# Performance work log

Hardware: AMD Instinct MI355X
Metric: run time of the kernel (lower is better)

Reference implementation:

```python
import jax, jax.numpy as jnp
import numpy as np

B, T, C = 2, 2048, 1280
H, D = 10, 128  # n_head, head_dim (n_kv_head == n_head, so no repeat)
EPS = 1e-5
NEG = -1e9


def setup_inputs() -> dict:
    key = jax.random.key(0)
    ks = jax.random.split(key, 7)
    s = 0.02
    return {
        "x": jax.random.normal(ks[0], (B, T, C), jnp.float32),
        "cos": jax.random.normal(ks[1], (1, 1, T, D // 2), jnp.float32),
        "sin": jax.random.normal(ks[2], (1, 1, T, D // 2), jnp.float32),
        "Wq": jax.random.normal(ks[3], (C, C), jnp.float32) * s,
        "Wk": jax.random.normal(ks[4], (C, C), jnp.float32) * s,
        "Wv": jax.random.normal(ks[5], (C, C), jnp.float32) * s,
        "Wproj": jax.random.normal(ks[6], (C, C), jnp.float32) * s,
    }


def _rope(x, cos, sin):
    # x: [b,h,t,d]; split last dim in half
    x1, x2 = jnp.split(x, 2, axis=-1)
    y1 = x1 * cos + x2 * sin
    y2 = -x1 * sin + x2 * cos
    return jnp.concatenate([y1, y2], axis=-1)


def _rms_norm(x):
    mean = jnp.mean(x * x, axis=-1, keepdims=True)
    return x / jnp.sqrt(mean + EPS)


def reference(x, cos, sin, Wq, Wk, Wv, Wproj):
    b, t, c = x.shape
    # nn.Linear: y = x @ W.T; weights stored [out, in]
    q = (x @ Wq.T).reshape(b, t, H, D).transpose(0, 2, 1, 3)  # [b,h,t,d]
    k = (x @ Wk.T).reshape(b, t, H, D).transpose(0, 2, 1, 3)
    v = (x @ Wv.T).reshape(b, t, H, D).transpose(0, 2, 1, 3)
    q = _rms_norm(_rope(q, cos, sin))
    k = _rms_norm(_rope(k, cos, sin))
    scale = 1.0 / jnp.sqrt(jnp.float32(D))
    scores = jnp.einsum("bhqd,bhkd->bhqk", q, k) * scale
    mask = jnp.triu(jnp.ones((t, t), scores.dtype), k=1)  # 1 above diagonal
    scores = scores + mask * NEG
    attn = jax.nn.softmax(scores, axis=-1)
    y = jnp.einsum("bhqk,bhkd->bhqd", attn, v)
    y = y.transpose(0, 2, 1, 3).reshape(b, t, c)
    return y @ Wproj.T
```

## Files before the change

### kernel.cpp

```cpp
#include <hip/hip_runtime.h>
#include <hip/hip_bf16.h>

#define B_ 2
#define T_ 2048
#define C_ 1280
#define H_ 10
#define D_ 128
#define BT_ (B_*T_)

typedef __hip_bfloat16 bf16;
typedef __attribute__((ext_vector_type(8))) short short8;
typedef __attribute__((ext_vector_type(4))) float f32x4;

__device__ __forceinline__ float bf2f(bf16 v){ return __bfloat162float(v); }
__device__ __forceinline__ bf16  f2bf(float v){ return __float2bfloat16(v); }

struct alignas(8) bf4 { bf16 a,b,c,d; };

__device__ __forceinline__ void gl2lds(const bf16* g, bf16* l) {
    __builtin_amdgcn_global_load_lds(
        (const __attribute__((address_space(1))) void*)g,
        (__attribute__((address_space(3))) void*)l,
        16, 0, 0);
}

__global__ __launch_bounds__(256)
void cvtall(const float* __restrict__ x,  const float* __restrict__ w0,
            const float* __restrict__ w1, const float* __restrict__ w2,
            const float* __restrict__ w3, bf16* __restrict__ xb,
            bf16* __restrict__ wb)
{
    int bid = blockIdx.x;
    const float* s; bf16* d; int i;
    if (bid < 5120) {
        s = x; d = xb; i = (bid*256 + threadIdx.x)*4;
    } else {
        bid -= 5120;
        const int w = bid / 1600;
        const int r = bid % 1600;
        s = (w==0)?w0:(w==1)?w1:(w==2)?w2:w3;
        d = wb + (size_t)w*C_*C_;
        i = (r*256 + threadIdx.x)*4;
    }
    const float4 v = *(const float4*)(s + i);
    bf4 o = { f2bf(v.x), f2bf(v.y), f2bf(v.z), f2bf(v.w) };
    *(bf4*)(d + i) = o;
}

__global__ __launch_bounds__(256,4)
void gemm_qkv(const bf16* __restrict__ A, const bf16* __restrict__ Wb,
              bf16* __restrict__ q, bf16* __restrict__ k, bf16* __restrict__ vT,
              const float* __restrict__ cosp, const float* __restrict__ sinp)
{
    __shared__ __align__(16) bf16 smem[17408];
    bf16* As = smem;
    bf16* Bs = smem + 8192;
    const int z = blockIdx.z;
    const bf16* Wm = Wb + (size_t)z*C_*C_;
    const int wave = threadIdx.x >> 6;
    const int lane = threadIdx.x & 63;
    const int l15 = lane & 15, quad = lane >> 4;
    const int row0 = blockIdx.x*128;
    const int col0 = blockIdx.y*128;
    const int wm = (wave>>1)*64, wn = (wave&1)*64;
    const int srow = lane >> 3;
    const int scol = (lane & 7)*8;

    const f32x4 fzero = {0.f,0.f,0.f,0.f};
    f32x4 acc[4][4];
    #pragma unroll
    for (int i=0;i<4;i++)
        #pragma unroll
        for (int j=0;j<4;j++) acc[i][j] = fzero;

    const bf16* Ag = A  + (size_t)(row0 + wave*32 + srow)*C_ + scol;
    const bf16* Bg = Wm + (size_t)(col0 + wave*32 + srow)*C_ + scol;
    bf16* Al = As + (wave*32)*64;
    bf16* Bl = Bs + (wave*32)*64;

    for (int k0 = 0; k0 < C_; k0 += 64) {
        __syncthreads();
        #pragma unroll
        for (int i=0;i<4;i++){
            gl2lds(Ag + (size_t)i*8*C_ + k0, Al + i*8*64);
            gl2lds(Bg + (size_t)i*8*C_ + k0, Bl + i*8*64);
        }
        asm volatile("s_waitcnt vmcnt(0)" ::: "memory");
        __syncthreads();
        #pragma unroll
        for (int h=0; h<2; ++h) {
            short8 af[4], bfv[4];
            #pragma unroll
            for (int mt=0; mt<4; ++mt) af[mt]  = *(const short8*)(As + (wm + mt*16 + l15)*64 + h*32 + quad*8);
            #pragma unroll
            for (int nt=0; nt<4; ++nt) bfv[nt] = *(const short8*)(Bs + (wn + nt*16 + l15)*64 + h*32 + quad*8);
            #pragma unroll
            for (int mt=0; mt<4; ++mt)
                #pragma unroll
                for (int nt=0; nt<4; ++nt)
                    acc[mt][nt] = __builtin_amdgcn_mfma_f32_16x16x32_bf16(af[mt], bfv[nt], acc[mt][nt], 0,0,0);
        }
    }

    __syncthreads();
    if (z == 2) {
        const int RS = 136;
        #pragma unroll
        for (int mt=0; mt<4; ++mt)
            #pragma unroll
            for (int nt=0; nt<4; ++nt) {
                bf4 pk = { f2bf(acc[mt][nt][0]), f2bf(acc[mt][nt][1]),
                           f2bf(acc[mt][nt][2]), f2bf(acc[mt][nt][3]) };
                *(bf4*)(smem + (wn + nt*16 + l15)*RS + wm + mt*16 + quad*4) = pk;
            }
        __syncthreads();
        const int b    = row0 >> 11;
        const int trow = row0 & 2047;
        const int h    = col0 >> 7;
        bf16* vbase = vT + (size_t)(b*H_ + h)*D_*T_ + trow;
        const int g   = threadIdx.x >> 4;
        const int l16 = threadIdx.x & 15;
        #pragma unroll
        for (int i=0;i<8;i++){
            const int col = i*16 + g;
            *(short8*)(vbase + (size_t)col*T_ + l16*8) = *(const short8*)(smem + col*RS + l16*8);
        }
    } else {
        bf16* dst = z ? k : q;
        bf16* my  = smem + wave*4096;
        bf16* pr  = smem + (wave^1)*4096;
        float* ssb = (float*)(smem + 16384);
        #pragma unroll
        for (int mt=0; mt<4; ++mt)
            #pragma unroll
            for (int nt=0; nt<4; ++nt) {
                bf4 pk = { f2bf(acc[mt][nt][0]), f2bf(acc[mt][nt][1]),
                           f2bf(acc[mt][nt][2]), f2bf(acc[mt][nt][3]) };
                *(bf4*)(my + ((((mt*4+nt)*4+quad)*16+l15)<<2)) = pk;
            }
        __syncthreads();
        const bool upper = (wave & 1);
        float ss[4][4];
        #pragma unroll
        for (int mt=0; mt<4; ++mt) {
            #pragma unroll
            for (int r=0; r<4; ++r) ss[mt][r] = 0.f;
            #pragma unroll
            for (int nt=0; nt<4; ++nt) {
                const bf4 pv = *(const bf4*)(pr + ((((mt*4+nt)*4+quad)*16+l15)<<2));
                const float p[4] = { bf2f(pv.a), bf2f(pv.b), bf2f(pv.c), bf2f(pv.d) };
                const int j = nt*16 + l15;
                #pragma unroll
                for (int r=0; r<4; ++r) {
                    const int t = (row0 + wm + mt*16 + quad*4 + r) & 2047;
                    const float c = cosp[(size_t)t*64 + j];
                    const float s = sinp[(size_t)t*64 + j];
                    const float y = upper ? (acc[mt][nt][r]*c - p[r]*s)
                                          : (acc[mt][nt][r]*c + p[r]*s);
                    acc[mt][nt][r] = y;
                    ss[mt][r] += y*y;
                }
            }
            #pragma unroll
            for (int r=0; r<4; ++r) {
                #pragma unroll
                for (int off=1; off<16; off<<=1) ss[mt][r] += __shfl_xor(ss[mt][r], off);
            }
        }
        if (l15 == 0) {
            #pragma unroll
            for (int mt=0; mt<4; ++mt)
                #pragma unroll
                for (int r=0; r<4; ++r)
                    ssb[wave*64 + mt*16 + quad*4 + r] = ss[mt][r];
        }
        __syncthreads();
        #pragma unroll
        for (int mt=0; mt<4; ++mt)
            #pragma unroll
            for (int r=0; r<4; ++r) {
                const float sst = ss[mt][r] + ssb[(wave^1)*64 + mt*16 + quad*4 + r];
                const float sc = rsqrtf(sst*(1.0f/128.0f) + 1e-5f);
                #pragma unroll
                for (int nt=0; nt<4; ++nt)
                    dst[(size_t)(row0 + wm + mt*16 + quad*4 + r)*C_ + col0 + wn + nt*16 + l15]
                        = f2bf(acc[mt][nt][r]*sc);
            }
    }
}

__global__ __launch_bounds__(256,4)
void gemm_nt_m64(const bf16* __restrict__ A, const bf16* __restrict__ Wm,
                 float* __restrict__ Om)
{
    __shared__ __align__(16) bf16 As[64*64];
    __shared__ __align__(16) bf16 Bs[128*64];
    const int wave = threadIdx.x >> 6;
    const int lane = threadIdx.x & 63;
    const int l15 = lane & 15, quad = lane >> 4;
    const int row0 = blockIdx.x*64;
    const int col0 = blockIdx.y*128;
    const int wm = (wave>>1)*32, wn = (wave&1)*64;
    const int srow = lane >> 3;
    const int scol = (lane & 7)*8;

    const f32x4 fzero = {0.f,0.f,0.f,0.f};
    f32x4 acc[2][4];
    #pragma unroll
    for (int i=0;i<2;i++)
        #pragma unroll
        for (int j=0;j<4;j++) acc[i][j] = fzero;

    const bf16* Ag = A  + (size_t)(row0 + wave*16 + srow)*C_ + scol;
    const bf16* Bg = Wm + (size_t)(col0 + wave*32 + srow)*C_ + scol;
    bf16* Al = As + (wave*16)*64;
    bf16* Bl = Bs + (wave*32)*64;

    for (int k0 = 0; k0 < C_; k0 += 64) {
        __syncthreads();
        #pragma unroll
        for (int i=0;i<2;i++)
            gl2lds(Ag + (size_t)i*8*C_ + k0, Al + i*8*64);
        #pragma unroll
        for (int i=0;i<4;i++)
            gl2lds(Bg + (size_t)i*8*C_ + k0, Bl + i*8*64);
        asm volatile("s_waitcnt vmcnt(0)" ::: "memory");
        __syncthreads();
        #pragma unroll
        for (int h=0; h<2; ++h) {
            short8 af[2], bfv[4];
            #pragma unroll
            for (int mt=0; mt<2; ++mt) af[mt]  = *(const short8*)(As + (wm + mt*16 + l15)*64 + h*32 + quad*8);
            #pragma unroll
            for (int nt=0; nt<4; ++nt) bfv[nt] = *(const short8*)(Bs + (wn + nt*16 + l15)*64 + h*32 + quad*8);
            #pragma unroll
            for (int mt=0; mt<2; ++mt)
                #pragma unroll
                for (int nt=0; nt<4; ++nt)
                    acc[mt][nt] = __builtin_amdgcn_mfma_f32_16x16x32_bf16(af[mt], bfv[nt], acc[mt][nt], 0,0,0);
        }
    }
    #pragma unroll
    for (int mt=0; mt<2; ++mt)
        #pragma unroll
        for (int nt=0; nt<4; ++nt)
            #pragma unroll
            for (int r=0; r<4; ++r)
                Om[(size_t)(row0 + wm + mt*16 + quad*4 + r)*C_ + col0 + wn + nt*16 + l15] = acc[mt][nt][r];
}

#define M0_ 11.3137085f
__global__ __launch_bounds__(256,3)
void attn(const bf16* __restrict__ Q, const bf16* __restrict__ K,
          const bf16* __restrict__ Vt, bf16* __restrict__ Y,
          bf16* __restrict__ opart, float* __restrict__ lpart)
{
    __shared__ __align__(16) bf16 kbuf[64*128];
    __shared__ __align__(16) bf16 vbuf[128*64];
    __shared__ __align__(16) bf16 ptile[4][16*72];
    const int wave = threadIdx.x >> 6, lane = threadIdx.x & 63;
    const int l15 = lane & 15, quad = lane >> 4;
    const int bh = blockIdx.x % 20;
    const int u  = blockIdx.x / 20;
    int m, seg;
    if (u < 32)      { m = 31 - (u>>2); seg = u & 3; }
    else if (u < 56) { const int v2 = u-32; m = 23 - v2/3; seg = v2%3; }
    else if (u < 72) { const int v2 = u-56; m = 15 - (v2>>1); seg = v2&1; }
    else             { m = 7 - (u-72); seg = 0; }
    const int b = bh / H_, h = bh % H_;
    const int t0 = m*64;
    const int nch = m + 1;
    const int cbeg = seg*8;
    const int cend = min(cbeg+8, nch);
    const bool direct = (m < 8);
    const size_t base = (size_t)b*T_*C_ + (size_t)h*D_;
    const bf16* Kbh = K + base;
    const bf16* Vbh = Vt + (size_t)bh*D_*T_;
    const int t0w = t0 + wave*16;
    const float scale = 0.08838834764831845f;
    bf16* pt = ptile[wave];

    short8 qa[4];
    {
        const bf16* qp = Q + base + (size_t)(t0w + l15)*C_ + quad*8;
        #pragma unroll
        for (int kb4=0; kb4<4; ++kb4) qa[kb4] = *(const short8*)(qp + kb4*32);
    }
    const f32x4 fzero = {0.f,0.f,0.f,0.f};
    f32x4 o[8];
    #pragma unroll
    for (int dt=0; dt<8; ++dt) o[dt] = fzero;
    float lp[4] = {0.f,0.f,0.f,0.f};

    const int vr_off = lane >> 3;
    const int vu     = lane & 7;

    for (int ch=cbeg; ch<cend; ++ch) {
        const int k0 = ch*64;
        __syncthreads();
        #pragma unroll
        for (int j=0;j<4;j++){
            const int row = wave*16 + j*4 + quad;
            const int ugk = (l15 - row) & 15;
            gl2lds(Kbh + (size_t)(k0 + row)*C_ + ugk*8, &kbuf[(wave*16 + j*4)*128]);
        }
        #pragma unroll
        for (int j=0;j<4;j++){
            const int r  = wave*32 + j*8 + vr_off;
            const int ugv = (vu - r) & 7;
            gl2lds(Vbh + (size_t)r*T_ + k0 + ugv*8, &vbuf[(wave*32 + j*8)*64]);
        }
        asm volatile("s_waitcnt vmcnt(0)" ::: "memory");
        __syncthreads();

        f32x4 sc4[4];
        #pragma unroll
        for (int c=0;c<4;c++) sc4[c] = fzero;
        #pragma unroll
        for (int c=0;c<4;c++){
            short8 kf[4];
            #pragma unroll
            for (int kb4=0; kb4<4; ++kb4) {
                const int up = (kb4*4 + quad + l15) & 15;
                kf[kb4] = *(const short8*)(&kbuf[(c*16 + l15)*128 + up*8]);
            }
            #pragma unroll
            for (int kb4=0; kb4<4; ++kb4)
                sc4[c] = __builtin_amdgcn_mfma_f32_16x16x32_bf16(qa[kb4], kf[kb4], sc4[c], 0,0,0);
        }
        const bool lastc = (ch == nch-1);
        #pragma unroll
        for (int r=0; r<4; ++r) {
            const int rt = t0w + quad*4 + r;
            float v[4];
            #pragma unroll
            for (int c=0;c<4;c++) v[c] = sc4[c][r]*scale;
            if (lastc) {
                #pragma unroll
                for (int c=0;c<4;c++) if (k0 + c*16 + l15 > rt) v[c] = -1e30f;
            }
            float p[4];
            #pragma unroll
            for (int c=0;c<4;c++) p[c] = __expf(v[c] - M0_);
            lp[r] += (p[0]+p[1]) + (p[2]+p[3]);
            #pragma unroll
            for (int c=0;c<4;c++) pt[(quad*4+r)*72 + c*16 + l15] = f2bf(p[c]);
        }
        asm volatile("s_waitcnt lgkmcnt(0)" ::: "memory");
        short8 pa[2];
        #pragma unroll
        for (int ks=0; ks<2; ++ks)
            pa[ks] = *(const short8*)(pt + l15*72 + ks*32 + quad*8);
        #pragma unroll
        for (int dt=0; dt<8; ++dt) {
            #pragma unroll
            for (int ks=0; ks<2; ++ks) {
                const int up = (ks*4 + quad + l15) & 7;
                short8 vF = *(const short8*)(&vbuf[(dt*16 + l15)*64 + up*8]);
                o[dt] = __builtin_amdgcn_mfma_f32_16x16x32_bf16(pa[ks], vF, o[dt], 0,0,0);
            }
        }
    }

    #pragma unroll
    for (int r=0; r<4; ++r) {
        #pragma unroll
        for (int off=1; off<16; off<<=1) lp[r] += __shfl_xor(lp[r], off);
    }
    if (direct) {
        float li[4];
        #pragma unroll
        for (int r=0; r<4; ++r) li[r] = 1.0f/lp[r];
        #pragma unroll
        for (int dt=0; dt<8; ++dt)
            #pragma unroll
            for (int r=0; r<4; ++r)
                Y[base + (size_t)(t0w + quad*4 + r)*C_ + dt*16 + l15] = f2bf(o[dt][r]*li[r]);
    } else {
        const int off = (m<16) ? (m-8)*2 : (m<24) ? 16 + (m-16)*3 : 40 + (m-24)*4;
        const int slot = bh*72 + off + seg;
        bf16* ob = opart + (size_t)slot*8192 + (wave*16)*128;
        #pragma unroll
        for (int dt=0; dt<8; ++dt)
            #pragma unroll
            for (int r=0; r<4; ++r)
                ob[(quad*4+r)*128 + dt*16 + l15] = f2bf(o[dt][r]);
        if (l15 == 0) {
            #pragma unroll
            for (int r=0; r<4; ++r) lpart[(size_t)slot*64 + wave*16 + quad*4 + r] = lp[r];
        }
    }
}

__global__ __launch_bounds__(256)
void combineN(const bf16* __restrict__ opart, const float* __restrict__ lpart,
              bf16* __restrict__ Y)
{
    const int tt = blockIdx.x;
    const int bh = tt / 24;
    const int m  = 8 + (tt % 24);
    const int nseg = (m + 8) >> 3;
    const int off = (m<16) ? (m-8)*2 : (m<24) ? 16 + (m-16)*3 : 40 + (m-24)*4;
    const int slot0 = bh*72 + off;
    const int b = bh / H_, h = bh % H_;
    const int row = threadIdx.x >> 2;
    const int d0 = (threadIdx.x & 3)*32;
    float l = 0.f;
    for (int s=0; s<nseg; ++s) l += lpart[(size_t)(slot0+s)*64 + row];
    const float li = 1.0f/l;
    float acc[32];
    #pragma unroll
    for (int e=0;e<32;e++) acc[e] = 0.f;
    for (int s=0; s<nseg; ++s) {
        const bf16* p = opart + (size_t)(slot0+s)*8192 + row*128 + d0;
        #pragma unroll
        for (int e=0;e<32;e++) acc[e] += bf2f(p[e]);
    }
    bf16 ov[32];
    #pragma unroll
    for (int e=0;e<32;e++) ov[e] = f2bf(acc[e]*li);
    bf16* yp = Y + (size_t)b*T_*C_ + (size_t)(m*64+row)*C_ + (size_t)h*D_ + d0;
    #pragma unroll
    for (int v=0; v<4; ++v) *(short8*)(yp + v*8) = *(const short8*)(&ov[v*8]);
}

extern "C" void kernel_launch(void* const* d_in, const int* in_sizes, int n_in,
                              void* d_out, int out_size, void* d_ws, size_t ws_size,
                              hipStream_t stream)
{
    const float* x    = (const float*)d_in[0];
    const float* cosp = (const float*)d_in[1];
    const float* sinp = (const float*)d_in[2];
    const float* Wq   = (const float*)d_in[3];
    const float* Wk   = (const float*)d_in[4];
    const float* Wv   = (const float*)d_in[5];
    const float* Wp   = (const float*)d_in[6];
    float* out = (float*)d_out;

    const size_t NE = (size_t)BT_ * C_;
    const size_t NW = (size_t)C_ * C_;
    bf16* xb = (bf16*)d_ws;
    bf16* wb = xb + NE;
    bf16* q  = wb + 4*NW;
    bf16* k  = q + NE;
    bf16* v  = k + NE;
    bf16* y  = v + NE;
    bf16* vT = y + NE;
    bf16* op = vT + NE;
    float* lpart = (float*)(op + (size_t)1440*8192);

    cvtall<<<dim3(11520), 256, 0, stream>>>(x, Wq, Wk, Wv, Wp, xb, wb);
    gemm_qkv<<<dim3(BT_/128, C_/128, 3), 256, 0, stream>>>(xb, wb, q, k, vT, cosp, sinp);
    attn<<<dim3(1600), 256, 0, stream>>>(q, k, vT, y, op, lpart);
    combineN<<<dim3(480), 256, 0, stream>>>(op, lpart, y);
    gemm_nt_m64<<<dim3(BT_/64, C_/128), 256, 0, stream>>>(y, wb + 3*NW, out);
}
```

Before: 232.3 us.

## Enlarge attention query tiles to 128 rows and do RoPE in registers

The attention kernel now gives each wave 32 query rows in two 16-row groups instead of 16, so the block covers 128 rows. Each K/V fragment loaded from LDS feeds two MFMAs, which halves LDS reads of K and V per query row. The key-range split and the combine kernel are reworked to match: 4-chunk segments, 1440 blocks and new slot offsets. In the QKV GEMM the column-to-wave mapping changes so each wave holds both RoPE halves, which removes the LDS exchange and one barrier. The cost is more accumulator registers per wave in attention, which may lower occupancy, and a more complex work split.

```diff
diff --git a/kernel.cpp b/kernel.cpp
--- a/kernel.cpp
+++ b/kernel.cpp
@@ -62,7 +62,8 @@
     const int l15 = lane & 15, quad = lane >> 4;
     const int row0 = blockIdx.x*128;
     const int col0 = blockIdx.y*128;
-    const int wm = (wave>>1)*64, wn = (wave&1)*64;
+    const int wm = (wave>>1)*64;
+    const int wn2 = (wave&1)*32;
     const int srow = lane >> 3;
     const int scol = (lane & 7)*8;
 
@@ -93,7 +94,10 @@
             #pragma unroll
             for (int mt=0; mt<4; ++mt) af[mt]  = *(const short8*)(As + (wm + mt*16 + l15)*64 + h*32 + quad*8);
             #pragma unroll
-            for (int nt=0; nt<4; ++nt) bfv[nt] = *(const short8*)(Bs + (wn + nt*16 + l15)*64 + h*32 + quad*8);
+            for (int nt=0; nt<4; ++nt) {
+                const int bc = wn2 + (nt&1)*16 + (nt>>1)*64;
+                bfv[nt] = *(const short8*)(Bs + (bc + l15)*64 + h*32 + quad*8);
+            }
             #pragma unroll
             for (int mt=0; mt<4; ++mt)
                 #pragma unroll
@@ -109,9 +113,10 @@
         for (int mt=0; mt<4; ++mt)
             #pragma unroll
             for (int nt=0; nt<4; ++nt) {
+                const int bc = wn2 + (nt&1)*16 + (nt>>1)*64;
                 bf4 pk = { f2bf(acc[mt][nt][0]), f2bf(acc[mt][nt][1]),
                            f2bf(acc[mt][nt][2]), f2bf(acc[mt][nt][3]) };
-                *(bf4*)(smem + (wn + nt*16 + l15)*RS + wm + mt*16 + quad*4) = pk;
+                *(bf4*)(smem + (bc + l15)*RS + wm + mt*16 + quad*4) = pk;
             }
         __syncthreads();
         const int b    = row0 >> 11;
@@ -127,38 +132,27 @@
         }
     } else {
         bf16* dst = z ? k : q;
-        bf16* my  = smem + wave*4096;
-        bf16* pr  = smem + (wave^1)*4096;
         float* ssb = (float*)(smem + 16384);
-        #pragma unroll
-        for (int mt=0; mt<4; ++mt)
-            #pragma unroll
-            for (int nt=0; nt<4; ++nt) {
-                bf4 pk = { f2bf(acc[mt][nt][0]), f2bf(acc[mt][nt][1]),
-                           f2bf(acc[mt][nt][2]), f2bf(acc[mt][nt][3]) };
-                *(bf4*)(my + ((((mt*4+nt)*4+quad)*16+l15)<<2)) = pk;
-            }
-        __syncthreads();
-        const bool upper = (wave & 1);
         float ss[4][4];
         #pragma unroll
         for (int mt=0; mt<4; ++mt) {
             #pragma unroll
             for (int r=0; r<4; ++r) ss[mt][r] = 0.f;
             #pragma unroll
-            for (int nt=0; nt<4; ++nt) {
-                const bf4 pv = *(const bf4*)(pr + ((((mt*4+nt)*4+quad)*16+l15)<<2));
-                const float p[4] = { bf2f(pv.a), bf2f(pv.b), bf2f(pv.c), bf2f(pv.d) };
-                const int j = nt*16 + l15;
+            for (int nt=0; nt<2; ++nt) {
+                const int j = wn2 + nt*16 + l15;
                 #pragma unroll
                 for (int r=0; r<4; ++r) {
                     const int t = (row0 + wm + mt*16 + quad*4 + r) & 2047;
                     const float c = cosp[(size_t)t*64 + j];
                     const float s = sinp[(size_t)t*64 + j];
-                    const float y = upper ? (acc[mt][nt][r]*c - p[r]*s)
-                                          : (acc[mt][nt][r]*c + p[r]*s);
-                    acc[mt][nt][r] = y;
-                    ss[mt][r] += y*y;
+                    const float a1 = acc[mt][nt][r];
+                    const float a2 = acc[mt][nt+2][r];
+                    const float y1 =  a1*c + a2*s;
+                    const float y2 =  a2*c - a1*s;
+                    acc[mt][nt][r]   = y1;
+                    acc[mt][nt+2][r] = y2;
+                    ss[mt][r] += y1*y1 + y2*y2;
                 }
             }
             #pragma unroll
@@ -182,9 +176,11 @@
                 const float sst = ss[mt][r] + ssb[(wave^1)*64 + mt*16 + quad*4 + r];
                 const float sc = rsqrtf(sst*(1.0f/128.0f) + 1e-5f);
                 #pragma unroll
-                for (int nt=0; nt<4; ++nt)
-                    dst[(size_t)(row0 + wm + mt*16 + quad*4 + r)*C_ + col0 + wn + nt*16 + l15]
+                for (int nt=0; nt<4; ++nt) {
+                    const int bc = wn2 + (nt&1)*16 + (nt>>1)*64;
+                    dst[(size_t)(row0 + wm + mt*16 + quad*4 + r)*C_ + col0 + bc + l15]
                         = f2bf(acc[mt][nt][r]*sc);
+                }
             }
     }
 }
@@ -257,40 +253,45 @@
 {
     __shared__ __align__(16) bf16 kbuf[64*128];
     __shared__ __align__(16) bf16 vbuf[128*64];
-    __shared__ __align__(16) bf16 ptile[4][16*72];
+    __shared__ __align__(16) bf16 ptile[4][32*72];
     const int wave = threadIdx.x >> 6, lane = threadIdx.x & 63;
     const int l15 = lane & 15, quad = lane >> 4;
     const int bh = blockIdx.x % 20;
-    const int u  = blockIdx.x / 20;
-    int m, seg;
-    if (u < 32)      { m = 31 - (u>>2); seg = u & 3; }
-    else if (u < 56) { const int v2 = u-32; m = 23 - v2/3; seg = v2%3; }
-    else if (u < 72) { const int v2 = u-56; m = 15 - (v2>>1); seg = v2&1; }
-    else             { m = 7 - (u-72); seg = 0; }
+    int u = blockIdx.x / 20;
+    int mp = 0, seg = 0;
+    for (int mm = 15; mm >= 0; --mm) {
+        const int ns = (mm + 2) >> 1;
+        if (u < ns) { mp = mm; seg = u; break; }
+        u -= ns;
+    }
     const int b = bh / H_, h = bh % H_;
-    const int t0 = m*64;
-    const int nch = m + 1;
-    const int cbeg = seg*8;
-    const int cend = min(cbeg+8, nch);
-    const bool direct = (m < 8);
+    const int t0 = mp*128;
+    const int nch = 2*mp + 2;
+    const int cbeg = seg*4;
+    const int cend = min(cbeg+4, nch);
+    const int dch = 2*mp + (wave>>1);
+    const bool direct = (mp < 2);
     const size_t base = (size_t)b*T_*C_ + (size_t)h*D_;
     const bf16* Kbh = K + base;
     const bf16* Vbh = Vt + (size_t)bh*D_*T_;
-    const int t0w = t0 + wave*16;
+    const int t0w = t0 + wave*32;
     const float scale = 0.08838834764831845f;
     bf16* pt = ptile[wave];
 
-    short8 qa[4];
-    {
-        const bf16* qp = Q + base + (size_t)(t0w + l15)*C_ + quad*8;
-        #pragma unroll
-        for (int kb4=0; kb4<4; ++kb4) qa[kb4] = *(const short8*)(qp + kb4*32);
+    short8 qa[2][4];
+    #pragma unroll
+    for (int rg=0; rg<2; ++rg) {
+        const bf16* qp = Q + base + (size_t)(t0w + rg*16 + l15)*C_ + quad*8;
+        #pragma unroll
+        for (int kb4=0; kb4<4; ++kb4) qa[rg][kb4] = *(const short8*)(qp + kb4*32);
     }
     const f32x4 fzero = {0.f,0.f,0.f,0.f};
-    f32x4 o[8];
-    #pragma unroll
-    for (int dt=0; dt<8; ++dt) o[dt] = fzero;
-    float lp[4] = {0.f,0.f,0.f,0.f};
+    f32x4 o[2][8];
+    #pragma unroll
+    for (int rg=0; rg<2; ++rg)
+        #pragma unroll
+        for (int dt=0; dt<8; ++dt) o[rg][dt] = fzero;
+    float lp[2][4] = {{0.f,0.f,0.f,0.f},{0.f,0.f,0.f,0.f}};
 
     const int vr_off = lane >> 3;
     const int vu     = lane & 7;
@@ -313,9 +314,11 @@
         asm volatile("s_waitcnt vmcnt(0)" ::: "memory");
         __syncthreads();
 
-        f32x4 sc4[4];
-        #pragma unroll
-        for (int c=0;c<4;c++) sc4[c] = fzero;
+        f32x4 sc4[2][4];
+        #pragma unroll
+        for (int rg=0; rg<2; ++rg)
+            #pragma unroll
+            for (int c=0;c<4;c++) sc4[rg][c] = fzero;
         #pragma unroll
         for (int c=0;c<4;c++){
             short8 kf[4];
@@ -325,69 +328,89 @@
                 kf[kb4] = *(const short8*)(&kbuf[(c*16 + l15)*128 + up*8]);
             }
             #pragma unroll
-            for (int kb4=0; kb4<4; ++kb4)
-                sc4[c] = __builtin_amdgcn_mfma_f32_16x16x32_bf16(qa[kb4], kf[kb4], sc4[c], 0,0,0);
-        }
-        const bool lastc = (ch == nch-1);
-        #pragma unroll
-        for (int r=0; r<4; ++r) {
-            const int rt = t0w + quad*4 + r;
-            float v[4];
-            #pragma unroll
-            for (int c=0;c<4;c++) v[c] = sc4[c][r]*scale;
-            if (lastc) {
-                #pragma unroll
-                for (int c=0;c<4;c++) if (k0 + c*16 + l15 > rt) v[c] = -1e30f;
-            }
-            float p[4];
-            #pragma unroll
-            for (int c=0;c<4;c++) p[c] = __expf(v[c] - M0_);
-            lp[r] += (p[0]+p[1]) + (p[2]+p[3]);
-            #pragma unroll
-            for (int c=0;c<4;c++) pt[(quad*4+r)*72 + c*16 + l15] = f2bf(p[c]);
+            for (int kb4=0; kb4<4; ++kb4) {
+                sc4[0][c] = __builtin_amdgcn_mfma_f32_16x16x32_bf16(qa[0][kb4], kf[kb4], sc4[0][c], 0,0,0);
+                sc4[1][c] = __builtin_amdgcn_mfma_f32_16x16x32_bf16(qa[1][kb4], kf[kb4], sc4[1][c], 0,0,0);
+            }
+        }
+        const bool maskc = (ch >= dch);
+        #pragma unroll
+        for (int rg=0; rg<2; ++rg) {
+            #pragma unroll
+            for (int r=0; r<4; ++r) {
+                const int rt = t0w + rg*16 + quad*4 + r;
+                float v[4];
+                #pragma unroll
+                for (int c=0;c<4;c++) v[c] = sc4[rg][c][r]*scale;
+                if (maskc) {
+                    #pragma unroll
+                    for (int c=0;c<4;c++) if (k0 + c*16 + l15 > rt) v[c] = -1e30f;
+                }
+                float p[4];
+                #pragma unroll
+                for (int c=0;c<4;c++) p[c] = __expf(v[c] - M0_);
+                lp[rg][r] += (p[0]+p[1]) + (p[2]+p[3]);
+                #pragma unroll
+                for (int c=0;c<4;c++) pt[(rg*16 + quad*4 + r)*72 + c*16 + l15] = f2bf(p[c]);
+            }
         }
         asm volatile("s_waitcnt lgkmcnt(0)" ::: "memory");
-        short8 pa[2];
-        #pragma unroll
-        for (int ks=0; ks<2; ++ks)
-            pa[ks] = *(const short8*)(pt + l15*72 + ks*32 + quad*8);
+        short8 pa[2][2];
+        #pragma unroll
+        for (int rg=0; rg<2; ++rg)
+            #pragma unroll
+            for (int ks=0; ks<2; ++ks)
+                pa[rg][ks] = *(const short8*)(pt + (rg*16 + l15)*72 + ks*32 + quad*8);
         #pragma unroll
         for (int dt=0; dt<8; ++dt) {
             #pragma unroll
             for (int ks=0; ks<2; ++ks) {
                 const int up = (ks*4 + quad + l15) & 7;
                 short8 vF = *(const short8*)(&vbuf[(dt*16 + l15)*64 + up*8]);
-                o[dt] = __builtin_amdgcn_mfma_f32_16x16x32_bf16(pa[ks], vF, o[dt], 0,0,0);
-            }
-        }
-    }
-
-    #pragma unroll
-    for (int r=0; r<4; ++r) {
-        #pragma unroll
-        for (int off=1; off<16; off<<=1) lp[r] += __shfl_xor(lp[r], off);
-    }
+                o[0][dt] = __builtin_amdgcn_mfma_f32_16x16x32_bf16(pa[0][ks], vF, o[0][dt], 0,0,0);
+                o[1][dt] = __builtin_amdgcn_mfma_f32_16x16x32_bf16(pa[1][ks], vF, o[1][dt], 0,0,0);
+            }
+        }
+    }
+
+    #pragma unroll
+    for (int rg=0; rg<2; ++rg)
+        #pragma unroll
+        for (int r=0; r<4; ++r) {
+            #pragma unroll
+            for (int off=1; off<16; off<<=1) lp[rg][r] += __shfl_xor(lp[rg][r], off);
+        }
     if (direct) {
-        float li[4];
-        #pragma unroll
-        for (int r=0; r<4; ++r) li[r] = 1.0f/lp[r];
-        #pragma unroll
-        for (int dt=0; dt<8; ++dt)
-            #pragma unroll
-            for (int r=0; r<4; ++r)
-                Y[base + (size_t)(t0w + quad*4 + r)*C_ + dt*16 + l15] = f2bf(o[dt][r]*li[r]);
+        float li[2][4];
+        #pragma unroll
+        for (int rg=0; rg<2; ++rg)
+            #pragma unroll
+            for (int r=0; r<4; ++r) li[rg][r] = 1.0f/lp[rg][r];
+        #pragma unroll
+        for (int rg=0; rg<2; ++rg)
+            #pragma unroll
+            for (int dt=0; dt<8; ++dt)
+                #pragma unroll
+                for (int r=0; r<4; ++r)
+                    Y[base + (size_t)(t0w + rg*16 + quad*4 + r)*C_ + dt*16 + l15] = f2bf(o[rg][dt][r]*li[rg][r]);
     } else {
-        const int off = (m<16) ? (m-8)*2 : (m<24) ? 16 + (m-16)*3 : 40 + (m-24)*4;
-        const int slot = bh*72 + off + seg;
-        bf16* ob = opart + (size_t)slot*8192 + (wave*16)*128;
-        #pragma unroll
-        for (int dt=0; dt<8; ++dt)
-            #pragma unroll
-            for (int r=0; r<4; ++r)
-                ob[(quad*4+r)*128 + dt*16 + l15] = f2bf(o[dt][r]);
+        int off = 0;
+        for (int j = 2; j < mp; ++j) off += (j+2)>>1;
+        const int slot = bh*70 + off + seg;
+        bf16* ob = opart + (size_t)slot*16384;
+        #pragma unroll
+        for (int rg=0; rg<2; ++rg)
+            #pragma unroll
+            for (int dt=0; dt<8; ++dt)
+                #pragma unroll
+                for (int r=0; r<4; ++r)
+                    ob[(size_t)(wave*32 + rg*16 + quad*4 + r)*128 + dt*16 + l15] = f2bf(o[rg][dt][r]);
         if (l15 == 0) {
             #pragma unroll
-            for (int r=0; r<4; ++r) lpart[(size_t)slot*64 + wave*16 + quad*4 + r] = lp[r];
+            for (int rg=0; rg<2; ++rg)
+                #pragma unroll
+                for (int r=0; r<4; ++r)
+                    lpart[(size_t)slot*128 + wave*32 + rg*16 + quad*4 + r] = lp[rg][r];
         }
     }
 }
@@ -397,31 +420,32 @@
               bf16* __restrict__ Y)
 {
     const int tt = blockIdx.x;
-    const int bh = tt / 24;
-    const int m  = 8 + (tt % 24);
-    const int nseg = (m + 8) >> 3;
-    const int off = (m<16) ? (m-8)*2 : (m<24) ? 16 + (m-16)*3 : 40 + (m-24)*4;
-    const int slot0 = bh*72 + off;
+    const int bh = tt / 14;
+    const int mp = 2 + (tt % 14);
+    const int nseg = (mp + 2) >> 1;
+    int off = 0;
+    for (int j = 2; j < mp; ++j) off += (j+2)>>1;
+    const int slot0 = bh*70 + off;
     const int b = bh / H_, h = bh % H_;
-    const int row = threadIdx.x >> 2;
-    const int d0 = (threadIdx.x & 3)*32;
+    const int row = threadIdx.x >> 1;
+    const int d0 = (threadIdx.x & 1)*64;
     float l = 0.f;
-    for (int s=0; s<nseg; ++s) l += lpart[(size_t)(slot0+s)*64 + row];
+    for (int s=0; s<nseg; ++s) l += lpart[(size_t)(slot0+s)*128 + row];
     const float li = 1.0f/l;
-    float acc[32];
-    #pragma unroll
-    for (int e=0;e<32;e++) acc[e] = 0.f;
+    float acc[64];
+    #pragma unroll
+    for (int e=0;e<64;e++) acc[e] = 0.f;
     for (int s=0; s<nseg; ++s) {
-        const bf16* p = opart + (size_t)(slot0+s)*8192 + row*128 + d0;
-        #pragma unroll
-        for (int e=0;e<32;e++) acc[e] += bf2f(p[e]);
-    }
-    bf16 ov[32];
-    #pragma unroll
-    for (int e=0;e<32;e++) ov[e] = f2bf(acc[e]*li);
-    bf16* yp = Y + (size_t)b*T_*C_ + (size_t)(m*64+row)*C_ + (size_t)h*D_ + d0;
-    #pragma unroll
-    for (int v=0; v<4; ++v) *(short8*)(yp + v*8) = *(const short8*)(&ov[v*8]);
+        const bf16* p = opart + (size_t)(slot0+s)*16384 + row*128 + d0;
+        #pragma unroll
+        for (int e=0;e<64;e++) acc[e] += bf2f(p[e]);
+    }
+    bf16 ov[64];
+    #pragma unroll
+    for (int e=0;e<64;e++) ov[e] = f2bf(acc[e]*li);
+    bf16* yp = Y + (size_t)b*T_*C_ + (size_t)(mp*128+row)*C_ + (size_t)h*D_ + d0;
+    #pragma unroll
+    for (int v=0; v<8; ++v) *(short8*)(yp + v*8) = *(const short8*)(&ov[v*8]);
 }
 
 extern "C" void kernel_launch(void* const* d_in, const int* in_sizes, int n_in,
@@ -443,15 +467,14 @@
     bf16* wb = xb + NE;
     bf16* q  = wb + 4*NW;
     bf16* k  = q + NE;
-    bf16* v  = k + NE;
-    bf16* y  = v + NE;
+    bf16* y  = k + NE;
     bf16* vT = y + NE;
     bf16* op = vT + NE;
-    float* lpart = (float*)(op + (size_t)1440*8192);
+    float* lpart = (float*)(op + (size_t)1400*16384);
 
     cvtall<<<dim3(11520), 256, 0, stream>>>(x, Wq, Wk, Wv, Wp, xb, wb);
     gemm_qkv<<<dim3(BT_/128, C_/128, 3), 256, 0, stream>>>(xb, wb, q, k, vT, cosp, sinp);
-    attn<<<dim3(1600), 256, 0, stream>>>(q, k, vT, y, op, lpart);
-    combineN<<<dim3(480), 256, 0, stream>>>(op, lpart, y);
+    attn<<<dim3(1440), 256, 0, stream>>>(q, k, vT, y, op, lpart);
+    combineN<<<dim3(280), 256, 0, stream>>>(op, lpart, y);
     gemm_nt_m64<<<dim3(BT_/64, C_/128), 256, 0, stream>>>(y, wb + 3*NW, out);
 }
```

After: 294.7 us. 26.9% more time.
